# Optimization experiments

Measured on AMD Instinct MI355X. Metric: run time of the kernel, lower is better.

Reference implementation:

```python
import jax, jax.numpy as jnp
import numpy as np

B, S, D = 4, 4096, 1024

def setup_inputs() -> dict:
    key = jax.random.key(0)
    k1, k2 = jax.random.split(key)
    x = jax.random.normal(k1, (B, S, D), dtype=jnp.float32)
    W_qkv = jax.random.normal(k2, (D, 3 * D), dtype=jnp.float32) * (D ** -0.5)
    b_qkv = jnp.zeros((3 * D,), dtype=jnp.float32)
    return {"x": x, "W_qkv": W_qkv, "b_qkv": b_qkv}

def reference(x, W_qkv, b_qkv):
    # qkv projection: [B,S,3D]
    qkv = jnp.einsum('bsd,de->bse', x, W_qkv) + b_qkv
    q, k, v = jnp.split(qkv, 3, axis=-1)  # each [B,S,D]
    scale = q.shape[-1] ** -0.5
    # full [B,S,S] score matrix, as in the original (non-fused) implementation
    scores = jnp.einsum('bqd,bkd->bqk', q, k) * scale
    attn = jax.nn.softmax(scores, axis=-1)
    out = jnp.einsum('bqk,bkd->bqd', attn, v)
    return out
```

## Files before the change

### kernel.cpp

```cpp
#include <hip/hip_runtime.h>
#include <math.h>

typedef unsigned short ushort_t;
typedef __attribute__((ext_vector_type(8))) short short8;
typedef __attribute__((ext_vector_type(4))) float floatx4;

#define VMCNT(n) asm volatile("s_waitcnt vmcnt(" #n ")" ::: "memory")

__device__ inline ushort_t f2bf(float x) {
    union { float f; unsigned int u; } c; c.f = x;
    unsigned int r = (c.u + 0x7fffu + ((c.u >> 16) & 1u)) >> 16;
    return (ushort_t)r;
}

__device__ __forceinline__ void glds16(const ushort_t* g, ushort_t* l) {
    __builtin_amdgcn_global_load_lds(
        (const __attribute__((address_space(1))) unsigned int*)g,
        (__attribute__((address_space(3))) unsigned int*)l,
        16, 0, 0);
}

__device__ __forceinline__ unsigned swzo(unsigned off) {
    return off ^ ((off >> 3) & 0x70u);
}

__global__ __launch_bounds__(256)
void wt_kernel(const float* __restrict__ W, ushort_t* __restrict__ Wt)
{
    __shared__ float tile[64][65];
    const int k0 = blockIdx.x * 64;
    const int n0 = blockIdx.y * 64;
    const int tid = threadIdx.x;
    #pragma unroll
    for (int ii = 0; ii < 16; ++ii) {
        int idx = ii * 256 + tid;
        int r = idx >> 6, c = idx & 63;
        tile[r][c] = W[(size_t)(k0 + r) * 3072 + n0 + c];
    }
    __syncthreads();
    #pragma unroll
    for (int ii = 0; ii < 16; ++ii) {
        int idx = ii * 256 + tid;
        int r = idx >> 6, c = idx & 63;
        Wt[(size_t)(n0 + r) * 1024 + k0 + c] = f2bf(tile[c][r]);
    }
}

__global__ __launch_bounds__(256)
void xcvt(const float* __restrict__ x, ushort_t* __restrict__ xb)
{
    const int i = (blockIdx.x * 256 + threadIdx.x) * 8;
    float4 f0 = *(const float4*)(x + i);
    float4 f1 = *(const float4*)(x + i + 4);
    ushort_t tmp[8] __attribute__((aligned(16)));
    tmp[0]=f2bf(f0.x); tmp[1]=f2bf(f0.y); tmp[2]=f2bf(f0.z); tmp[3]=f2bf(f0.w);
    tmp[4]=f2bf(f1.x); tmp[5]=f2bf(f1.y); tmp[6]=f2bf(f1.z); tmp[7]=f2bf(f1.w);
    *(uint4*)(xb + i) = *(const uint4*)tmp;
}

__global__ __launch_bounds__(256)
void qkv_mfma(const float* __restrict__ x, const ushort_t* __restrict__ Wt,
              const float* __restrict__ bias,
              ushort_t* __restrict__ q, ushort_t* __restrict__ k,
              ushort_t* __restrict__ vt)
{
    __shared__ ushort_t As[128][72];
    __shared__ ushort_t Bs[128][72];
    const int tid = threadIdx.x;
    const int w = tid >> 6, lane = tid & 63;
    const int m = lane & 15, quad = lane >> 4;
    const int col0 = blockIdx.x * 128;
    const int r0   = blockIdx.y * 128;

    floatx4 o[2][8];
    #pragma unroll
    for (int rf = 0; rf < 2; ++rf)
        #pragma unroll
        for (int nf = 0; nf < 8; ++nf)
            o[rf][nf] = (floatx4){0.f, 0.f, 0.f, 0.f};

    for (int kc = 0; kc < 16; ++kc) {
        const int kdim = kc * 64;
        __syncthreads();
        #pragma unroll
        for (int ii = 0; ii < 4; ++ii) {
            int lin = ii * 256 + tid;
            int row = lin >> 3, seg = lin & 7;
            const float* src = x + (size_t)(r0 + row) * 1024 + kdim + seg * 8;
            float4 f0 = *(const float4*)src;
            float4 f1 = *(const float4*)(src + 4);
            ushort_t tmp[8] __attribute__((aligned(16)));
            tmp[0]=f2bf(f0.x); tmp[1]=f2bf(f0.y); tmp[2]=f2bf(f0.z); tmp[3]=f2bf(f0.w);
            tmp[4]=f2bf(f1.x); tmp[5]=f2bf(f1.y); tmp[6]=f2bf(f1.z); tmp[7]=f2bf(f1.w);
            *(uint4*)&As[row][seg * 8] = *(const uint4*)tmp;
        }
        #pragma unroll
        for (int ii = 0; ii < 4; ++ii) {
            int lin = ii * 256 + tid;
            int row = lin >> 3, seg = lin & 7;
            const ushort_t* src = Wt + (size_t)(col0 + row) * 1024 + kdim + seg * 8;
            *(uint4*)&Bs[row][seg * 8] = *(const uint4*)src;
        }
        __syncthreads();
        #pragma unroll
        for (int kk = 0; kk < 2; ++kk) {
            short8 af[2];
            #pragma unroll
            for (int rf = 0; rf < 2; ++rf)
                af[rf] = *(const short8*)&As[w * 32 + rf * 16 + m][kk * 32 + quad * 8];
            #pragma unroll
            for (int nf = 0; nf < 8; ++nf) {
                short8 bf = *(const short8*)&Bs[nf * 16 + m][kk * 32 + quad * 8];
                #pragma unroll
                for (int rf = 0; rf < 2; ++rf)
                    o[rf][nf] = __builtin_amdgcn_mfma_f32_16x16x32_bf16(af[rf], bf, o[rf][nf], 0, 0, 0);
            }
        }
    }

    const int which = col0 >> 10;
    const int dbase = col0 & 1023;
    float bias_v[8];
    #pragma unroll
    for (int nf = 0; nf < 8; ++nf) bias_v[nf] = bias[col0 + nf * 16 + m];

    #pragma unroll
    for (int rf = 0; rf < 2; ++rf) {
        #pragma unroll
        for (int e = 0; e < 4; ++e) {
            const int g = r0 + w * 32 + rf * 16 + quad * 4 + e;
            #pragma unroll
            for (int nf = 0; nf < 8; ++nf) {
                const int c = dbase + nf * 16 + m;
                float val = o[rf][nf][e] + bias_v[nf];
                if (which == 0) {
                    q[(size_t)g * 1024 + c] = f2bf(val * 0.03125f);
                } else if (which == 1) {
                    k[(size_t)g * 1024 + c] = f2bf(val);
                } else {
                    vt[(size_t)(g >> 12) * 4194304 + (size_t)c * 4096 + (g & 4095)] = f2bf(val);
                }
            }
        }
    }
}

__global__ __launch_bounds__(256)
void qkv_mfma2(const ushort_t* __restrict__ xb, const ushort_t* __restrict__ Wt,
               const float* __restrict__ bias,
               ushort_t* __restrict__ q, ushort_t* __restrict__ k,
               ushort_t* __restrict__ vt)
{
    __shared__ __align__(1024) ushort_t smem[2 * 128 * 64];
    ushort_t (*As)[64] = (ushort_t (*)[64])smem;
    ushort_t (*Bs)[64] = (ushort_t (*)[64])(smem + 128 * 64);
    const int tid = threadIdx.x;
    const int w = tid >> 6, lane = tid & 63;
    const int m = lane & 15, quad = lane >> 4;
    const int lx = lane ^ ((lane >> 3) & 7);
    const int sr = lx >> 3, sc = (lx & 7) * 8;
    const int col0 = blockIdx.x * 128;
    const int r0   = blockIdx.y * 128;

    floatx4 o[2][8];
    #pragma unroll
    for (int rf = 0; rf < 2; ++rf)
        #pragma unroll
        for (int nf = 0; nf < 8; ++nf)
            o[rf][nf] = (floatx4){0.f, 0.f, 0.f, 0.f};

    for (int kc = 0; kc < 16; ++kc) {
        const int kdim = kc * 64;
        __syncthreads();
        #pragma unroll
        for (int ii = 0; ii < 4; ++ii) {
            glds16(xb + (size_t)(r0 + w * 32 + ii * 8 + sr) * 1024 + kdim + sc,
                   &As[w * 32 + ii * 8][0]);
            glds16(Wt + (size_t)(col0 + w * 32 + ii * 8 + sr) * 1024 + kdim + sc,
                   &Bs[w * 32 + ii * 8][0]);
        }
        __syncthreads();
        #pragma unroll
        for (int kk = 0; kk < 2; ++kk) {
            short8 af[2];
            #pragma unroll
            for (int rf = 0; rf < 2; ++rf)
                af[rf] = *(const short8*)((const char*)As +
                          swzo((unsigned)((w * 32 + rf * 16 + m) * 128 + kk * 64 + quad * 16)));
            #pragma unroll
            for (int nf = 0; nf < 8; ++nf) {
                short8 bf = *(const short8*)((const char*)Bs +
                          swzo((unsigned)((nf * 16 + m) * 128 + kk * 64 + quad * 16)));
                #pragma unroll
                for (int rf = 0; rf < 2; ++rf)
                    o[rf][nf] = __builtin_amdgcn_mfma_f32_16x16x32_bf16(af[rf], bf, o[rf][nf], 0, 0, 0);
            }
        }
    }

    const int which = col0 >> 10;
    const int dbase = col0 & 1023;
    float bias_v[8];
    #pragma unroll
    for (int nf = 0; nf < 8; ++nf) bias_v[nf] = bias[col0 + nf * 16 + m];

    if (which == 2) {
        const size_t voffb = (size_t)(r0 >> 12) * 4194304;
        const int grow0 = r0 & 4095;
        ushort_t (*T)[136] = (ushort_t (*)[136])smem;
        #pragma unroll
        for (int p = 0; p < 2; ++p) {
            __syncthreads();
            #pragma unroll
            for (int rf = 0; rf < 2; ++rf)
                #pragma unroll
                for (int e = 0; e < 4; ++e) {
                    const int row = w * 32 + rf * 16 + quad * 4 + e;
                    #pragma unroll
                    for (int nn = 0; nn < 4; ++nn) {
                        const int nf = p * 4 + nn;
                        T[nn * 16 + m][row] = f2bf(o[rf][nf][e] + bias_v[nf]);
                    }
                }
            __syncthreads();
            #pragma unroll
            for (int ii = 0; ii < 4; ++ii) {
                int idx = ii * 256 + tid;
                int c = idx >> 4, seg = idx & 15;
                *(uint4*)&vt[voffb + (size_t)(dbase + p * 64 + c) * 4096 + grow0 + seg * 8]
                    = *(const uint4*)&T[c][seg * 8];
            }
        }
    } else {
        #pragma unroll
        for (int rf = 0; rf < 2; ++rf) {
            #pragma unroll
            for (int e = 0; e < 4; ++e) {
                const int g = r0 + w * 32 + rf * 16 + quad * 4 + e;
                #pragma unroll
                for (int nf = 0; nf < 8; ++nf) {
                    const int c = dbase + nf * 16 + m;
                    float val = o[rf][nf][e] + bias_v[nf];
                    if (which == 0) {
                        q[(size_t)g * 1024 + c] = f2bf(val * 0.03125f);
                    } else {
                        k[(size_t)g * 1024 + c] = f2bf(val);
                    }
                }
            }
        }
    }
}

__global__ __launch_bounds__(512, 2)
void fused_attn(const ushort_t* __restrict__ q, const ushort_t* __restrict__ kb_,
                const ushort_t* __restrict__ vt, float* __restrict__ out)
{
    __shared__ __align__(1024) unsigned char lds[141312];
    ushort_t (*Qs)[128][32] = (ushort_t(*)[128][32])(lds);
    ushort_t (*Ks)[256][32] = (ushort_t(*)[256][32])(lds + 24576);
    ushort_t (*Pls)[264]    = (ushort_t(*)[264])(lds);
    ushort_t (*Vs)[512][32] = (ushort_t(*)[512][32])(lds + 73728);
    float    (*redL)[4]     = (float(*)[4])(lds + 139264);

    const int tid  = threadIdx.x;
    const int w    = tid >> 6, lane = tid & 63;
    const int m    = lane & 15, quad = lane >> 4;
    const int wr   = w & 1, wc = w >> 1;
    const int lx   = lane ^ ((lane >> 3) & 7);
    const int lr   = lx >> 2, lc = (lx & 3) * 8;
    const int bid  = blockIdx.x;
    const int b    = (bid & 7) >> 1;
    const int n    = ((bid >> 3) << 1) | (bid & 1);
    const int n0x  = (n >> 5) * 512;
    const int r0   = (n & 31) * 128;
    const size_t qoff = (size_t)b * 4096 * 1024;
    const size_t voff = (size_t)b * 4194304;

    unsigned qof[4], kof[4], vof[8];
    #pragma unroll
    for (int i = 0; i < 4; ++i)
        qof[i] = swzo((unsigned)((wr * 64 + i * 16 + m) * 64 + quad * 16));
    #pragma unroll
    for (int j = 0; j < 4; ++j)
        kof[j] = swzo((unsigned)((wc * 64 + j * 16 + m) * 64 + quad * 16));
    #pragma unroll
    for (int j = 0; j < 8; ++j)
        vof[j] = swzo((unsigned)((wc * 128 + j * 16 + m) * 64 + quad * 16));

    const ushort_t* qsrc  = q   + qoff + (size_t)(r0 + w * 16 + lr) * 1024 + lc;
    const ushort_t* ksrc0 = kb_ + qoff + (size_t)(w * 32 + lr) * 1024 + lc;
    const ushort_t* ksrc1 = kb_ + qoff + (size_t)(w * 32 + 16 + lr) * 1024 + lc;

    floatx4 o[4][8];
    #pragma unroll
    for (int i = 0; i < 4; ++i)
        #pragma unroll
        for (int j = 0; j < 8; ++j)
            o[i][j] = (floatx4){0.f, 0.f, 0.f, 0.f};
    float lsum[4] = {};

    for (int kt = 0; kt < 16; ++kt) {
        const int kbase = kt * 256;

        floatx4 s[4][4];
        #pragma unroll
        for (int j = 0; j < 4; ++j)
            #pragma unroll
            for (int i = 0; i < 4; ++i)
                s[j][i] = (floatx4){0.f, 0.f, 0.f, 0.f};

        glds16(qsrc,                        &Qs[0][w * 16][0]);
        glds16(ksrc0 + (size_t)kbase * 1024, &Ks[0][w * 32][0]);
        glds16(ksrc1 + (size_t)kbase * 1024, &Ks[0][w * 32 + 16][0]);
        {
            int cur = 0;
            for (int kc = 0; kc < 32; ++kc) {
                if (kc < 31) {
                    const int nxt = (cur == 2) ? 0 : cur + 1;
                    const int kd = (kc + 1) * 32;
                    glds16(qsrc + kd,                             &Qs[nxt][w * 16][0]);
                    glds16(ksrc0 + (size_t)kbase * 1024 + kd,     &Ks[nxt][w * 32][0]);
                    glds16(ksrc1 + (size_t)kbase * 1024 + kd,     &Ks[nxt][w * 32 + 16][0]);
                    VMCNT(3);
                } else {
                    VMCNT(0);
                }
                __builtin_amdgcn_s_barrier();
                __builtin_amdgcn_sched_barrier(0);
                short8 af[4], bf[4];
                #pragma unroll
                for (int i = 0; i < 4; ++i)
                    af[i] = *(const short8*)((const char*)Qs[cur] + qof[i]);
                #pragma unroll
                for (int j = 0; j < 4; ++j)
                    bf[j] = *(const short8*)((const char*)Ks[cur] + kof[j]);
                __builtin_amdgcn_s_setprio(1);
                #pragma unroll
                for (int j = 0; j < 4; ++j)
                    #pragma unroll
                    for (int i = 0; i < 4; ++i)
                        s[j][i] = __builtin_amdgcn_mfma_f32_16x16x32_bf16(bf[j], af[i], s[j][i], 0, 0, 0);
                __builtin_amdgcn_s_setprio(0);
                cur = (cur == 2) ? 0 : cur + 1;
            }
        }
        __syncthreads();

        #pragma unroll
        for (int i = 0; i < 4; ++i)
            #pragma unroll
            for (int j = 0; j < 4; ++j) {
                float p0 = __expf(s[j][i][0]);
                float p1 = __expf(s[j][i][1]);
                float p2 = __expf(s[j][i][2]);
                float p3 = __expf(s[j][i][3]);
                lsum[i] += (p0 + p1) + (p2 + p3);
                unsigned lo = (unsigned)f2bf(p0) | ((unsigned)f2bf(p1) << 16);
                unsigned hi = (unsigned)f2bf(p2) | ((unsigned)f2bf(p3) << 16);
                *(uint2*)&Pls[wr * 64 + i * 16 + m][wc * 64 + j * 16 + quad * 4] =
                    (uint2){lo, hi};
            }

        {
            #pragma unroll
            for (int i = 0; i < 4; ++i)
                glds16(vt + voff + (size_t)(n0x + w * 64 + i * 16 + lr) * 4096 + kbase + lc,
                       &Vs[0][w * 64 + i * 16][0]);
        }
        __syncthreads();

        for (int vc = 0; vc < 8; ++vc) {
            const int p = vc & 1;
            if (vc < 7) {
                const int kd = kbase + (vc + 1) * 32;
                #pragma unroll
                for (int i = 0; i < 4; ++i)
                    glds16(vt + voff + (size_t)(n0x + w * 64 + i * 16 + lr) * 4096 + kd + lc,
                           &Vs[p ^ 1][w * 64 + i * 16][0]);
            }
            short8 ap[4], bv[8];
            #pragma unroll
            for (int i = 0; i < 4; ++i)
                ap[i] = *(const short8*)&Pls[wr * 64 + i * 16 + m][vc * 32 + quad * 8];
            #pragma unroll
            for (int j = 0; j < 8; ++j)
                bv[j] = *(const short8*)((const char*)Vs[p] + vof[j]);
            __builtin_amdgcn_s_setprio(1);
            #pragma unroll
            for (int i = 0; i < 4; ++i)
                #pragma unroll
                for (int j = 0; j < 8; ++j)
                    o[i][j] = __builtin_amdgcn_mfma_f32_16x16x32_bf16(ap[i], bv[j], o[i][j], 0, 0, 0);
            __builtin_amdgcn_s_setprio(0);
            __syncthreads();
        }
    }

    #pragma unroll
    for (int i = 0; i < 4; ++i) {
        float l = lsum[i];
        l += __shfl_xor(l, 16);
        l += __shfl_xor(l, 32);
        if (quad == 0) redL[wr * 64 + i * 16 + m][wc] = l;
    }
    __syncthreads();
    #pragma unroll
    for (int i = 0; i < 4; ++i)
        #pragma unroll
        for (int e = 0; e < 4; ++e) {
            const int row = wr * 64 + i * 16 + quad * 4 + e;
            const float inv = 1.0f / (redL[row][0] + redL[row][1] + redL[row][2] + redL[row][3]);
            const int g = b * 4096 + r0 + row;
            #pragma unroll
            for (int j = 0; j < 8; ++j)
                out[(size_t)g * 1024 + n0x + wc * 128 + j * 16 + m] = o[i][j][e] * inv;
        }
}

extern "C" void kernel_launch(void* const* d_in, const int* in_sizes, int n_in,
                              void* d_out, int out_size, void* d_ws, size_t ws_size,
                              hipStream_t stream)
{
    const float* x    = (const float*)d_in[0];
    const float* W    = (const float*)d_in[1];
    const float* bias = (const float*)d_in[2];
    float* out = (float*)d_out;

    const size_t SZQ  = (size_t)4 * 4096 * 1024 * 2;
    const size_t SZWT = (size_t)3072 * 1024 * 2;
    const size_t SZXB = (size_t)4 * 4096 * 1024 * 2;
    const size_t NEED  = 3 * SZQ + SZWT;
    const size_t NEED2 = NEED + SZXB;
    if (ws_size < NEED) return;

    ushort_t* q  = (ushort_t*)d_ws;
    ushort_t* k  = (ushort_t*)((char*)d_ws + SZQ);
    ushort_t* vt = (ushort_t*)((char*)d_ws + 2 * SZQ);
    ushort_t* Wt = (ushort_t*)((char*)d_ws + 3 * SZQ);
    ushort_t* xb = (ushort_t*)((char*)d_ws + NEED);

    wt_kernel <<<dim3(16, 48),   256, 0, stream>>>(W, Wt);
    if (ws_size >= NEED2) {
        xcvt      <<<dim3(8192),    256, 0, stream>>>(x, xb);
        qkv_mfma2 <<<dim3(24, 128), 256, 0, stream>>>(xb, Wt, bias, q, k, vt);
    } else {
        qkv_mfma  <<<dim3(24, 128), 256, 0, stream>>>(x, Wt, bias, q, k, vt);
    }
    fused_attn<<<dim3(256), 512, 0, stream>>>(q, k, vt, out);
}
```

Before: 688.0 us.

## Widen QK^T k-chunks to 64 with double-buffered LDS staging

The QK^T stage now stages Q and K tiles in 64-wide d-chunks instead of 32-wide ones, and replaces the 3-stage ring buffer with a 2-stage double buffer. This halves the number of chunk iterations and barriers, and each chunk now feeds twice as many MFMAs. The cost is a larger LDS footprint (the LDS layout is reshuffled, with redL moved) and a full vmcnt(0) wait at the end of each chunk, which may expose load latency where the previous ring buffer hid it with partial waits. The larger LDS use may also prevent two blocks from fitting per CU.

Measured after the change: 778.3 us. 1.13x slower.

```diff
diff --git a/kernel.cpp b/kernel.cpp
--- a/kernel.cpp
+++ b/kernel.cpp
@@ -256,19 +256,20 @@
 void fused_attn(const ushort_t* __restrict__ q, const ushort_t* __restrict__ kb_,
                 const ushort_t* __restrict__ vt, float* __restrict__ out)
 {
-    __shared__ __align__(1024) unsigned char lds[141312];
-    ushort_t (*Qs)[128][32] = (ushort_t(*)[128][32])(lds);
-    ushort_t (*Ks)[256][32] = (ushort_t(*)[256][32])(lds + 24576);
+    __shared__ __align__(1024) unsigned char lds[163840];
+    ushort_t (*Qs)[128][64] = (ushort_t(*)[128][64])(lds);
+    ushort_t (*Ks)[256][64] = (ushort_t(*)[256][64])(lds + 32768);
     ushort_t (*Pls)[264]    = (ushort_t(*)[264])(lds);
-    ushort_t (*Vs)[512][32] = (ushort_t(*)[512][32])(lds + 73728);
-    float    (*redL)[4]     = (float(*)[4])(lds + 139264);
+    ushort_t (*Vs)[512][32] = (ushort_t(*)[512][32])(lds + 98304);
+    float    (*redL)[4]     = (float(*)[4])(lds + 67584);
 
     const int tid  = threadIdx.x;
     const int w    = tid >> 6, lane = tid & 63;
     const int m    = lane & 15, quad = lane >> 4;
     const int wr   = w & 1, wc = w >> 1;
     const int lx   = lane ^ ((lane >> 3) & 7);
-    const int lr   = lx >> 2, lc = (lx & 3) * 8;
+    const int lr   = lx >> 2, lc  = (lx & 3) * 8;
+    const int lrA  = lx >> 3, lcA = (lx & 7) * 8;
     const int bid  = blockIdx.x;
     const int b    = (bid & 7) >> 1;
     const int n    = ((bid >> 3) << 1) | (bid & 1);
@@ -277,20 +278,23 @@
     const size_t qoff = (size_t)b * 4096 * 1024;
     const size_t voff = (size_t)b * 4194304;
 
-    unsigned qof[4], kof[4], vof[8];
+    unsigned qof[4][2], kof[4][2], vof[8];
     #pragma unroll
     for (int i = 0; i < 4; ++i)
-        qof[i] = swzo((unsigned)((wr * 64 + i * 16 + m) * 64 + quad * 16));
+        #pragma unroll
+        for (int ks = 0; ks < 2; ++ks)
+            qof[i][ks] = swzo((unsigned)((wr * 64 + i * 16 + m) * 128 + ks * 64 + quad * 16));
     #pragma unroll
     for (int j = 0; j < 4; ++j)
-        kof[j] = swzo((unsigned)((wc * 64 + j * 16 + m) * 64 + quad * 16));
+        #pragma unroll
+        for (int ks = 0; ks < 2; ++ks)
+            kof[j][ks] = swzo((unsigned)((wc * 64 + j * 16 + m) * 128 + ks * 64 + quad * 16));
     #pragma unroll
     for (int j = 0; j < 8; ++j)
         vof[j] = swzo((unsigned)((wc * 128 + j * 16 + m) * 64 + quad * 16));
 
-    const ushort_t* qsrc  = q   + qoff + (size_t)(r0 + w * 16 + lr) * 1024 + lc;
-    const ushort_t* ksrc0 = kb_ + qoff + (size_t)(w * 32 + lr) * 1024 + lc;
-    const ushort_t* ksrc1 = kb_ + qoff + (size_t)(w * 32 + 16 + lr) * 1024 + lc;
+    const ushort_t* qsrc = q   + qoff + (size_t)(r0 + w * 16 + lrA) * 1024 + lcA;
+    const ushort_t* ksrc = kb_ + qoff + (size_t)(w * 32 + lrA) * 1024 + lcA;
 
     floatx4 o[4][8];
     #pragma unroll
@@ -302,6 +306,7 @@
 
     for (int kt = 0; kt < 16; ++kt) {
         const int kbase = kt * 256;
+        const ushort_t* kptr = ksrc + (size_t)kbase * 1024;
 
         floatx4 s[4][4];
         #pragma unroll
@@ -310,42 +315,50 @@
             for (int i = 0; i < 4; ++i)
                 s[j][i] = (floatx4){0.f, 0.f, 0.f, 0.f};
 
-        glds16(qsrc,                        &Qs[0][w * 16][0]);
-        glds16(ksrc0 + (size_t)kbase * 1024, &Ks[0][w * 32][0]);
-        glds16(ksrc1 + (size_t)kbase * 1024, &Ks[0][w * 32 + 16][0]);
-        {
-            int cur = 0;
-            for (int kc = 0; kc < 32; ++kc) {
-                if (kc < 31) {
-                    const int nxt = (cur == 2) ? 0 : cur + 1;
-                    const int kd = (kc + 1) * 32;
-                    glds16(qsrc + kd,                             &Qs[nxt][w * 16][0]);
-                    glds16(ksrc0 + (size_t)kbase * 1024 + kd,     &Ks[nxt][w * 32][0]);
-                    glds16(ksrc1 + (size_t)kbase * 1024 + kd,     &Ks[nxt][w * 32 + 16][0]);
-                    VMCNT(3);
-                } else {
-                    VMCNT(0);
-                }
-                __builtin_amdgcn_s_barrier();
-                __builtin_amdgcn_sched_barrier(0);
-                short8 af[4], bf[4];
-                #pragma unroll
-                for (int i = 0; i < 4; ++i)
-                    af[i] = *(const short8*)((const char*)Qs[cur] + qof[i]);
-                #pragma unroll
-                for (int j = 0; j < 4; ++j)
-                    bf[j] = *(const short8*)((const char*)Ks[cur] + kof[j]);
-                __builtin_amdgcn_s_setprio(1);
+        #pragma unroll
+        for (int ii = 0; ii < 2; ++ii)
+            glds16(qsrc + ii * 8192, &Qs[0][w * 16 + ii * 8][0]);
+        #pragma unroll
+        for (int ii = 0; ii < 4; ++ii)
+            glds16(kptr + ii * 8192, &Ks[0][w * 32 + ii * 8][0]);
+        VMCNT(0);
+        __builtin_amdgcn_s_barrier();
+        __builtin_amdgcn_sched_barrier(0);
+        for (int kc = 0; kc < 16; ++kc) {
+            const int cur = kc & 1;
+            if (kc < 15) {
+                const int kd = (kc + 1) * 64;
+                #pragma unroll
+                for (int ii = 0; ii < 2; ++ii)
+                    glds16(qsrc + ii * 8192 + kd, &Qs[cur ^ 1][w * 16 + ii * 8][0]);
+                #pragma unroll
+                for (int ii = 0; ii < 4; ++ii)
+                    glds16(kptr + ii * 8192 + kd, &Ks[cur ^ 1][w * 32 + ii * 8][0]);
+            }
+            short8 af[4][2], bf[4][2];
+            #pragma unroll
+            for (int i = 0; i < 4; ++i)
+                #pragma unroll
+                for (int ks = 0; ks < 2; ++ks)
+                    af[i][ks] = *(const short8*)((const char*)Qs[cur] + qof[i][ks]);
+            #pragma unroll
+            for (int j = 0; j < 4; ++j)
+                #pragma unroll
+                for (int ks = 0; ks < 2; ++ks)
+                    bf[j][ks] = *(const short8*)((const char*)Ks[cur] + kof[j][ks]);
+            __builtin_amdgcn_s_setprio(1);
+            #pragma unroll
+            for (int ks = 0; ks < 2; ++ks)
                 #pragma unroll
                 for (int j = 0; j < 4; ++j)
                     #pragma unroll
                     for (int i = 0; i < 4; ++i)
-                        s[j][i] = __builtin_amdgcn_mfma_f32_16x16x32_bf16(bf[j], af[i], s[j][i], 0, 0, 0);
-                __builtin_amdgcn_s_setprio(0);
-                cur = (cur == 2) ? 0 : cur + 1;
-            }
-        }
-        __syncthreads();
+                        s[j][i] = __builtin_amdgcn_mfma_f32_16x16x32_bf16(bf[j][ks], af[i][ks], s[j][i], 0, 0, 0);
+            __builtin_amdgcn_s_setprio(0);
+            VMCNT(0);
+            __builtin_amdgcn_s_barrier();
+            __builtin_amdgcn_sched_barrier(0);
+        }
 
         #pragma unroll
         for (int i = 0; i < 4; ++i)
```
